# Kernel optimization log

Measured on AMD Instinct MI355X. Metric: run time of the kernel, lower is better.

Reference implementation:

```python
import jax, jax.numpy as jnp
import numpy as np

NUM_EMBEDDINGS = 8192
EMBEDDING_DIM = 256
COMMITMENT_COST = 0.25


def setup_inputs() -> dict:
    key = jax.random.key(0)
    k1, k2 = jax.random.split(key)
    inputs = jax.random.normal(k1, (16, 2048, EMBEDDING_DIM), dtype=jnp.float32)
    # codebook initialized uniform(-1/K, 1/K) as in the torch module
    codebook = jax.random.uniform(
        k2, (NUM_EMBEDDINGS, EMBEDDING_DIM), dtype=jnp.float32,
        minval=-1.0 / NUM_EMBEDDINGS, maxval=1.0 / NUM_EMBEDDINGS)
    return {"inputs": inputs, "codebook": codebook}


def reference(inputs, codebook):
    B, T, D = inputs.shape
    flat = inputs.reshape(-1, D)                      # [BT, D]
    distances = (
        jnp.sum(flat * flat, axis=1, keepdims=True)
        + jnp.sum(codebook * codebook, axis=1)
        - 2.0 * jnp.matmul(flat, codebook.T)
    )
    idx = jnp.argmin(distances, axis=1)               # [BT]
    quantized = codebook[idx].reshape(B, T, D)        # gather == one-hot @ codebook
    e_latent_loss = jnp.mean((jax.lax.stop_gradient(quantized) - inputs) ** 2)
    q_latent_loss = jnp.mean((quantized - jax.lax.stop_gradient(inputs)) ** 2)
    loss = q_latent_loss + COMMITMENT_COST * e_latent_loss
    # straight-through estimator
    quantized_st = inputs + jax.lax.stop_gradient(quantized - inputs)
    return quantized_st, idx.reshape(B, T), loss
```

## Files before the change

### kernel.cpp

```cpp
#include <hip/hip_runtime.h>
#include <hip/hip_bf16.h>
#include <stdint.h>

#define D      256
#define K      8192
#define NROWS  32768
#define QELEMS 8388608

typedef __attribute__((ext_vector_type(8))) short bf16x8;
typedef __attribute__((ext_vector_type(4))) float f32x4;
typedef unsigned int u32;
typedef unsigned short u16;

__device__ __forceinline__ u16 f2bf(float f) {
    u32 b = __float_as_uint(f);
    return (u16)((b + 0x7fffu + ((b >> 16) & 1u)) >> 16);
}
__device__ __forceinline__ float bf2f(u16 h) {
    return __uint_as_float((u32)h << 16);
}

__global__ __launch_bounds__(256) void vq_prep_kernel(
    const float* __restrict__ cb, u16* __restrict__ ch,
    float* __restrict__ se, u16* __restrict__ seh, float* __restrict__ loss_sum) {
    int row = blockIdx.x * 4 + (threadIdx.x >> 6);
    int l = threadIdx.x & 63;
    float4 v = *(const float4*)(cb + (size_t)row * D + l * 4);
    ushort4 o;
    o.x = f2bf(v.x); o.y = f2bf(v.y); o.z = f2bf(v.z); o.w = f2bf(v.w);
    *(ushort4*)(ch + (size_t)row * D + l * 4) = o;
    float s = v.x * v.x + v.y * v.y + v.z * v.z + v.w * v.w;
    #pragma unroll
    for (int off = 32; off > 0; off >>= 1) s += __shfl_down(s, off, 64);
    if (l == 0) { se[row] = s; seh[row] = f2bf(s); }
    if (blockIdx.x == 0 && threadIdx.x == 0) *loss_sum = 0.f;
}

__global__ __launch_bounds__(512, 4) void vq_filter_kernel(
    const u16* __restrict__ ch, const float* __restrict__ x,
    const u16* __restrict__ seh, u32* __restrict__ cand)
{
    __shared__ union {
        u16 as[2][16384];
        struct { float mv[64 * 33]; u32 mc[64 * 33]; } mg;
    } S;
    __shared__ __align__(16) u16 seL[8192];

    const int tid  = threadIdx.x;
    const int lane = tid & 63;
    const int wave = tid >> 6;
    const int m_w  = wave & 3;
    const int n_w  = wave >> 2;
    const int l15  = lane & 15;
    const int l4   = lane >> 4;
    const int row0 = blockIdx.x * 64;

    {
        uint4* dl = (uint4*)seL;
        const uint4* sg = (const uint4*)seh;
        dl[tid] = sg[tid];
        dl[tid + 512] = sg[tid + 512];
    }

    bf16x8 Bf[2][8];
    #pragma unroll
    for (int nt = 0; nt < 2; ++nt) {
        const float* xr = x + (size_t)(row0 + n_w * 32 + nt * 16 + l15) * D + l4 * 8;
        #pragma unroll
        for (int c = 0; c < 8; ++c) {
            float4 a = *(const float4*)(xr + c * 32);
            float4 b = *(const float4*)(xr + c * 32 + 4);
            bf16x8 f;
            f[0] = (short)f2bf(a.x); f[1] = (short)f2bf(a.y);
            f[2] = (short)f2bf(a.z); f[3] = (short)f2bf(a.w);
            f[4] = (short)f2bf(b.x); f[5] = (short)f2bf(b.y);
            f[6] = (short)f2bf(b.z); f[7] = (short)f2bf(b.w);
            Bf[nt][c] = f;
        }
    }

    float b0[2], b1[2]; int c0[2], c1[2];
    #pragma unroll
    for (int nt = 0; nt < 2; ++nt) { b0[nt] = 1e30f; b1[nt] = 1e30f; c0[nt] = 0; c1[nt] = 0; }

#define STAGE(TILE, BUF) do {                                                 \
    const int _kn = (TILE) << 6;                                              \
    _Pragma("unroll")                                                         \
    for (int i = 0; i < 4; ++i) {                                             \
        const u16* gp = ch + (size_t)(_kn + i * 16 + l15) * D + wave * 32 + l4 * 8; \
        u16* lb = &S.as[(BUF)][(size_t)(wave * 4 + i) * 512];                 \
        __builtin_amdgcn_global_load_lds(                                     \
            (const __attribute__((address_space(1))) u32*)gp,                 \
            (__attribute__((address_space(3))) u32*)lb, 16, 0, 0);            \
    }                                                                         \
} while (0)

#define EPI(NT, A) do {                                                       \
    float t0 = fmaf(-2.f, (A)[0], _se0);                                      \
    float t1 = fmaf(-2.f, (A)[1], _se1);                                      \
    float t2 = fmaf(-2.f, (A)[2], _se2);                                      \
    float t3 = fmaf(-2.f, (A)[3], _se3);                                      \
    float tmn = fminf(fminf(t0, t1), fminf(t2, t3));                          \
    if (tmn < b1[NT]) {                                                       \
        float tv[4] = {t0, t1, t2, t3};                                       \
        _Pragma("unroll")                                                     \
        for (int r = 0; r < 4; ++r) {                                         \
            float t = tv[r];                                                  \
            int cv = _kt + m_w * 16 + l4 * 4 + r;                             \
            bool in0 = t < b0[NT];                                            \
            bool in1 = t < b1[NT];                                            \
            float ob0 = b0[NT]; int oc0 = c0[NT];                             \
            b1[NT] = in0 ? ob0 : (in1 ? t  : b1[NT]);                         \
            c1[NT] = in0 ? oc0 : (in1 ? cv : c1[NT]);                         \
            b0[NT] = in0 ? t  : ob0;                                          \
            c0[NT] = in0 ? cv : oc0;                                          \
        }                                                                     \
    }                                                                         \
} while (0)

#define BODY(T, DO_STAGE, VMN) do {                                           \
    if (DO_STAGE) STAGE((T) + 1, ((T) + 1) & 1);                              \
    asm volatile("s_waitcnt vmcnt(" #VMN ")" ::: "memory");                   \
    __builtin_amdgcn_s_barrier();                                             \
    const int _kt = (T) << 6;                                                 \
    const u16* _as = &S.as[(T) & 1][0];                                       \
    f32x4 acc0 = {0.f,0.f,0.f,0.f}, acc1 = {0.f,0.f,0.f,0.f};                 \
    _Pragma("unroll")                                                         \
    for (int c = 0; c < 8; ++c) {                                             \
        bf16x8 Af = *(const bf16x8*)(_as + (size_t)(c * 4 + m_w) * 512 + lane * 8); \
        acc0 = __builtin_amdgcn_mfma_f32_16x16x32_bf16(Af, Bf[0][c], acc0, 0, 0, 0); \
        acc1 = __builtin_amdgcn_mfma_f32_16x16x32_bf16(Af, Bf[1][c], acc1, 0, 0, 0); \
    }                                                                         \
    ushort4 _sh = *(const ushort4*)(seL + _kt + m_w * 16 + l4 * 4);           \
    float _se0 = bf2f(_sh.x), _se1 = bf2f(_sh.y);                             \
    float _se2 = bf2f(_sh.z), _se3 = bf2f(_sh.w);                             \
    EPI(0, acc0); EPI(1, acc1);                                               \
    __builtin_amdgcn_s_barrier();                                             \
} while (0)

    STAGE(0, 0);
    __syncthreads();

    #pragma unroll 1
    for (int t = 0; t < 127; ++t) BODY(t, 1, 4);
    BODY(127, 0, 0);

#undef BODY
#undef EPI
#undef STAGE

    #pragma unroll
    for (int nt = 0; nt < 2; ++nt) {
        int rl = n_w * 32 + nt * 16 + l15;
        int g  = m_w * 4 + l4;
        S.mg.mv[rl * 33 + g * 2]     = b0[nt];
        S.mg.mv[rl * 33 + g * 2 + 1] = b1[nt];
        S.mg.mc[rl * 33 + g * 2]     = (u32)c0[nt];
        S.mg.mc[rl * 33 + g * 2 + 1] = (u32)c1[nt];
    }
    __syncthreads();

    {
        int tsk = tid;
        int row = tsk >> 3, m = tsk & 7;
        const float* v  = S.mg.mv + row * 33 + m * 4;
        const u32*   cc = S.mg.mc + row * 33 + m * 4;
        float v00 = v[0],  v01 = v[1],  v10 = v[2],  v11 = v[3];
        u32   c00 = cc[0], c01 = cc[1], c10 = cc[2], c11 = cc[3];
        bool  aw  = v00 <= v10;
        u32   w0c = aw ? c00 : c10;
        float s1  = aw ? v10 : v00; u32 s1c = aw ? c10 : c00;
        float s2  = aw ? v01 : v11; u32 s2c = aw ? c01 : c11;
        u32   w1c = (s2 <= s1) ? s2c : s1c;
        cand[(size_t)(row0 + row) * 16 + m * 2]     = w0c;
        cand[(size_t)(row0 + row) * 16 + m * 2 + 1] = w1c;
    }
}

__global__ __launch_bounds__(1024) void vq_rescore_kernel(
    const float* __restrict__ x, const float* __restrict__ cb,
    const float* __restrict__ se, const u32* __restrict__ cand,
    float* __restrict__ out, float* __restrict__ loss_sum)
{
    const int wave = threadIdx.x >> 6;
    const int lane = threadIdx.x & 63;
    const int row  = blockIdx.x * 16 + wave;

    float4 xv = *(const float4*)(x + (size_t)row * D + lane * 4);
    float sx = xv.x * xv.x + xv.y * xv.y + xv.z * xv.z + xv.w * xv.w;
    #pragma unroll
    for (int o = 1; o < 64; o <<= 1) sx += __shfl_xor(sx, o, 64);

    u32 myc = cand[(size_t)row * 16 + (lane & 15)];
    float best = 1e30f; int bk = 0x7fffffff;
    #pragma unroll 4
    for (int j = 0; j < 16; ++j) {
        int code = __shfl((int)myc, j, 64);
        float4 ev = *(const float4*)(cb + (size_t)code * D + lane * 4);
        float p = xv.x * ev.x + xv.y * ev.y + xv.z * ev.z + xv.w * ev.w;
        #pragma unroll
        for (int o = 1; o < 64; o <<= 1) p += __shfl_xor(p, o, 64);
        float dist = (sx + se[code]) - 2.0f * p;
        if (dist < best || (dist == best && code < bk)) { best = dist; bk = code; }
    }

    float4 q = *(const float4*)(cb + (size_t)bk * D + lane * 4);
    *(float4*)(out + (size_t)row * D + lane * 4) = q;
    float dx = q.x - xv.x, dy = q.y - xv.y, dz = q.z - xv.z, dw = q.w - xv.w;
    float s = dx * dx + dy * dy + dz * dz + dw * dw;
    #pragma unroll
    for (int o = 1; o < 64; o <<= 1) s += __shfl_xor(s, o, 64);
    if (lane == 0) out[QELEMS + row] = (float)bk;

    __shared__ float red[16];
    if (lane == 0) red[wave] = s;
    __syncthreads();
    if (threadIdx.x == 0) {
        float t = 0.f;
        #pragma unroll
        for (int w2 = 0; w2 < 16; ++w2) t += red[w2];
        atomicAdd(loss_sum, t);
    }
}

__global__ void vq_fin_kernel(const float* __restrict__ loss_sum, float* __restrict__ out) {
    out[QELEMS + NROWS] = 1.25f * (*loss_sum) * (1.0f / (float)QELEMS);
}

extern "C" void kernel_launch(void* const* d_in, const int* in_sizes, int n_in,
                              void* d_out, int out_size, void* d_ws, size_t ws_size,
                              hipStream_t stream) {
    const float* x  = (const float*)d_in[0];
    const float* cb = (const float*)d_in[1];
    float* out = (float*)d_out;

    u16* ch = (u16*)d_out;

    char* ws = (char*)d_ws;
    float* loss_sum = (float*)ws;
    float* sebuf    = (float*)(ws + 4096);
    u16*   seh      = (u16*)(ws + 40960);
    u32*   cand     = (u32*)(ws + 65536);

    vq_prep_kernel<<<K / 4, 256, 0, stream>>>(cb, ch, sebuf, seh, loss_sum);
    vq_filter_kernel<<<NROWS / 64, 512, 0, stream>>>(ch, x, seh, cand);
    vq_rescore_kernel<<<NROWS / 16, 1024, 0, stream>>>(x, cb, sebuf, cand, out, loss_sum);
    vq_fin_kernel<<<1, 1, 0, stream>>>(loss_sum, out);
}
```

Measured before the change: 399.0 us.

## Split codebook search across two blocks per row tile to double grid parallelism

The filter kernel now launches twice as many blocks, with each pair covering the same 64 input rows but searching only one half of the 8192-entry codebook. Each block keeps top-2 candidates per 16-lane group and reduces them to 4 candidate pairs, writing 8 of the 16 candidate slots per row. This is meant to raise occupancy and hide latency on a grid that was only 512 blocks. The cost is that input rows are loaded and converted to bf16 twice, and the merged candidate set is coarser per half.

After: 415.2 us. +4.1%, slower.

```diff
diff --git a/kernel.cpp b/kernel.cpp
--- a/kernel.cpp
+++ b/kernel.cpp
@@ -44,7 +44,7 @@
         u16 as[2][16384];
         struct { float mv[64 * 33]; u32 mc[64 * 33]; } mg;
     } S;
-    __shared__ __align__(16) u16 seL[8192];
+    __shared__ __align__(16) u16 seL[4096];
 
     const int tid  = threadIdx.x;
     const int lane = tid & 63;
@@ -53,13 +53,16 @@
     const int n_w  = wave >> 2;
     const int l15  = lane & 15;
     const int l4   = lane >> 4;
-    const int row0 = blockIdx.x * 64;
+    const int g    = blockIdx.x;
+    const int half = (g & 7) >> 2;
+    const int rc   = (g >> 3) * 4 + (g & 3);
+    const int row0 = rc * 64;
+    const int kbase = half * 4096;
 
     {
         uint4* dl = (uint4*)seL;
-        const uint4* sg = (const uint4*)seh;
+        const uint4* sg = (const uint4*)(seh + kbase);
         dl[tid] = sg[tid];
-        dl[tid + 512] = sg[tid + 512];
     }
 
     bf16x8 Bf[2][8];
@@ -84,7 +87,7 @@
     for (int nt = 0; nt < 2; ++nt) { b0[nt] = 1e30f; b1[nt] = 1e30f; c0[nt] = 0; c1[nt] = 0; }
 
 #define STAGE(TILE, BUF) do {                                                 \
-    const int _kn = (TILE) << 6;                                              \
+    const int _kn = kbase + ((TILE) << 6);                                    \
     _Pragma("unroll")                                                         \
     for (int i = 0; i < 4; ++i) {                                             \
         const u16* gp = ch + (size_t)(_kn + i * 16 + l15) * D + wave * 32 + l4 * 8; \
@@ -106,7 +109,7 @@
         _Pragma("unroll")                                                     \
         for (int r = 0; r < 4; ++r) {                                         \
             float t = tv[r];                                                  \
-            int cv = _kt + m_w * 16 + l4 * 4 + r;                             \
+            int cv = kbase + _kt + m_w * 16 + l4 * 4 + r;                     \
             bool in0 = t < b0[NT];                                            \
             bool in1 = t < b1[NT];                                            \
             float ob0 = b0[NT]; int oc0 = c0[NT];                             \
@@ -142,8 +145,8 @@
     __syncthreads();
 
     #pragma unroll 1
-    for (int t = 0; t < 127; ++t) BODY(t, 1, 4);
-    BODY(127, 0, 0);
+    for (int t = 0; t < 63; ++t) BODY(t, 1, 4);
+    BODY(63, 0, 0);
 
 #undef BODY
 #undef EPI
@@ -152,28 +155,37 @@
     #pragma unroll
     for (int nt = 0; nt < 2; ++nt) {
         int rl = n_w * 32 + nt * 16 + l15;
-        int g  = m_w * 4 + l4;
-        S.mg.mv[rl * 33 + g * 2]     = b0[nt];
-        S.mg.mv[rl * 33 + g * 2 + 1] = b1[nt];
-        S.mg.mc[rl * 33 + g * 2]     = (u32)c0[nt];
-        S.mg.mc[rl * 33 + g * 2 + 1] = (u32)c1[nt];
+        int gq = m_w * 4 + l4;
+        S.mg.mv[rl * 33 + gq * 2]     = b0[nt];
+        S.mg.mv[rl * 33 + gq * 2 + 1] = b1[nt];
+        S.mg.mc[rl * 33 + gq * 2]     = (u32)c0[nt];
+        S.mg.mc[rl * 33 + gq * 2 + 1] = (u32)c1[nt];
     }
     __syncthreads();
 
-    {
-        int tsk = tid;
-        int row = tsk >> 3, m = tsk & 7;
-        const float* v  = S.mg.mv + row * 33 + m * 4;
-        const u32*   cc = S.mg.mc + row * 33 + m * 4;
-        float v00 = v[0],  v01 = v[1],  v10 = v[2],  v11 = v[3];
-        u32   c00 = cc[0], c01 = cc[1], c10 = cc[2], c11 = cc[3];
-        bool  aw  = v00 <= v10;
-        u32   w0c = aw ? c00 : c10;
-        float s1  = aw ? v10 : v00; u32 s1c = aw ? c10 : c00;
-        float s2  = aw ? v01 : v11; u32 s2c = aw ? c01 : c11;
-        u32   w1c = (s2 <= s1) ? s2c : s1c;
-        cand[(size_t)(row0 + row) * 16 + m * 2]     = w0c;
-        cand[(size_t)(row0 + row) * 16 + m * 2 + 1] = w1c;
+    if (tid < 256) {
+        int row = tid >> 2, q = tid & 3;
+        const float* v  = S.mg.mv + row * 33 + q * 8;
+        const u32*   cc = S.mg.mc + row * 33 + q * 8;
+        bool  a1 = v[0] <= v[2];
+        float p0v = a1 ? v[0] : v[2];  u32 p0c = a1 ? cc[0] : cc[2];
+        float s1a = a1 ? v[2] : v[0];  u32 s1ac = a1 ? cc[2] : cc[0];
+        float s2a = a1 ? v[1] : v[3];  u32 s2ac = a1 ? cc[1] : cc[3];
+        bool  a2 = s2a <= s1a;
+        float p1v = a2 ? s2a : s1a;    u32 p1c = a2 ? s2ac : s1ac;
+        bool  b1m = v[4] <= v[6];
+        float q0v = b1m ? v[4] : v[6]; u32 q0c = b1m ? cc[4] : cc[6];
+        float s1b = b1m ? v[6] : v[4]; u32 s1bc = b1m ? cc[6] : cc[4];
+        float s2b = b1m ? v[5] : v[7]; u32 s2bc = b1m ? cc[5] : cc[7];
+        bool  b2 = s2b <= s1b;
+        float q1v = b2 ? s2b : s1b;    u32 q1c = b2 ? s2bc : s1bc;
+        bool  f1 = p0v <= q0v;
+        u32   w0c = f1 ? p0c : q0c;
+        float s1f = f1 ? q0v : p0v;    u32 s1fc = f1 ? q0c : p0c;
+        float s2f = f1 ? p1v : q1v;    u32 s2fc = f1 ? p1c : q1c;
+        u32   w1c = (s2f <= s1f) ? s2fc : s1fc;
+        cand[(size_t)(row0 + row) * 16 + half * 8 + q * 2]     = w0c;
+        cand[(size_t)(row0 + row) * 16 + half * 8 + q * 2 + 1] = w1c;
     }
 }
 
@@ -243,7 +255,7 @@
     u32*   cand     = (u32*)(ws + 65536);
 
     vq_prep_kernel<<<K / 4, 256, 0, stream>>>(cb, ch, sebuf, seh, loss_sum);
-    vq_filter_kernel<<<NROWS / 64, 512, 0, stream>>>(ch, x, seh, cand);
+    vq_filter_kernel<<<2 * NROWS / 64, 512, 0, stream>>>(ch, x, seh, cand);
     vq_rescore_kernel<<<NROWS / 16, 1024, 0, stream>>>(x, cb, sebuf, cand, out, loss_sum);
     vq_fin_kernel<<<1, 1, 0, stream>>>(loss_sum, out);
 }
```

## Split codebook tiles into half-K phases with a four-slot LDS ring

Applied to the files above, without the earlier changes.

Each 64-code tile is now split into two half-depth phases. Each phase loads into one slot of a four-deep LDS ring and is prefetched three phases ahead, with one barrier per phase instead of two. LDS fragment reads are issued before the wait and barrier, and MFMA priority is raised with s_setprio, to overlap loads with compute. The early LDS reads happen before the matching vmcnt wait and barrier, and slot reuse is not clearly fenced, so the code risks reading stale tile data.

Measured after the change: 401.8 us. About the same (+0.7%).

```diff
diff --git a/kernel.cpp b/kernel.cpp
--- a/kernel.cpp
+++ b/kernel.cpp
@@ -41,7 +41,7 @@
     const u16* __restrict__ seh, u32* __restrict__ cand)
 {
     __shared__ union {
-        u16 as[2][16384];
+        u16 hb[4][8192];
         struct { float mv[64 * 33]; u32 mc[64 * 33]; } mg;
     } S;
     __shared__ __align__(16) u16 seL[8192];
@@ -83,12 +83,16 @@
     #pragma unroll
     for (int nt = 0; nt < 2; ++nt) { b0[nt] = 1e30f; b1[nt] = 1e30f; c0[nt] = 0; c1[nt] = 0; }
 
-#define STAGE(TILE, BUF) do {                                                 \
-    const int _kn = (TILE) << 6;                                              \
+#define STAGE_HALF(H, SLOT) do {                                              \
+    const int _h = (H);                                                       \
+    const int _t64 = (_h >> 1) * 64;                                          \
+    const int _db  = (_h & 1) * 128;                                          \
     _Pragma("unroll")                                                         \
-    for (int i = 0; i < 4; ++i) {                                             \
-        const u16* gp = ch + (size_t)(_kn + i * 16 + l15) * D + wave * 32 + l4 * 8; \
-        u16* lb = &S.as[(BUF)][(size_t)(wave * 4 + i) * 512];                 \
+    for (int i = 0; i < 2; ++i) {                                             \
+        const int g2 = wave * 2 + i;                                          \
+        const u16* gp = ch + (size_t)(_t64 + (g2 & 3) * 16 + l15) * D         \
+                           + _db + (g2 >> 2) * 32 + l4 * 8;                   \
+        u16* lb = &S.hb[(SLOT)][(size_t)g2 * 512];                            \
         __builtin_amdgcn_global_load_lds(                                     \
             (const __attribute__((address_space(1))) u32*)gp,                 \
             (__attribute__((address_space(3))) u32*)lb, 16, 0, 0);            \
@@ -118,36 +122,59 @@
     }                                                                         \
 } while (0)
 
-#define BODY(T, DO_STAGE, VMN) do {                                           \
-    if (DO_STAGE) STAGE((T) + 1, ((T) + 1) & 1);                              \
+#define PHASE(P, HH, DO_STAGE, VMN) do {                                      \
+    if (DO_STAGE) STAGE_HALF((P) + 3, ((P) + 3) & 3);                         \
+    const u16* _hb = &S.hb[(P) & 3][0];                                       \
+    bf16x8 Af0 = *(const bf16x8*)(_hb + (size_t)(0 * 4 + m_w) * 512 + lane * 8); \
+    bf16x8 Af1 = *(const bf16x8*)(_hb + (size_t)(1 * 4 + m_w) * 512 + lane * 8); \
+    bf16x8 Af2 = *(const bf16x8*)(_hb + (size_t)(2 * 4 + m_w) * 512 + lane * 8); \
+    bf16x8 Af3 = *(const bf16x8*)(_hb + (size_t)(3 * 4 + m_w) * 512 + lane * 8); \
     asm volatile("s_waitcnt vmcnt(" #VMN ")" ::: "memory");                   \
+    __builtin_amdgcn_sched_barrier(0);                                        \
     __builtin_amdgcn_s_barrier();                                             \
-    const int _kt = (T) << 6;                                                 \
-    const u16* _as = &S.as[(T) & 1][0];                                       \
-    f32x4 acc0 = {0.f,0.f,0.f,0.f}, acc1 = {0.f,0.f,0.f,0.f};                 \
-    _Pragma("unroll")                                                         \
-    for (int c = 0; c < 8; ++c) {                                             \
-        bf16x8 Af = *(const bf16x8*)(_as + (size_t)(c * 4 + m_w) * 512 + lane * 8); \
-        acc0 = __builtin_amdgcn_mfma_f32_16x16x32_bf16(Af, Bf[0][c], acc0, 0, 0, 0); \
-        acc1 = __builtin_amdgcn_mfma_f32_16x16x32_bf16(Af, Bf[1][c], acc1, 0, 0, 0); \
+    __builtin_amdgcn_sched_barrier(0);                                        \
+    asm volatile("s_waitcnt lgkmcnt(0)" ::: "memory");                        \
+    __builtin_amdgcn_sched_barrier(0);                                        \
+    if ((HH) == 0) { acc0 = (f32x4){0.f,0.f,0.f,0.f}; acc1 = (f32x4){0.f,0.f,0.f,0.f}; } \
+    __builtin_amdgcn_s_setprio(1);                                            \
+    acc0 = __builtin_amdgcn_mfma_f32_16x16x32_bf16(Af0, Bf[0][(HH)*4+0], acc0, 0, 0, 0); \
+    acc1 = __builtin_amdgcn_mfma_f32_16x16x32_bf16(Af0, Bf[1][(HH)*4+0], acc1, 0, 0, 0); \
+    acc0 = __builtin_amdgcn_mfma_f32_16x16x32_bf16(Af1, Bf[0][(HH)*4+1], acc0, 0, 0, 0); \
+    acc1 = __builtin_amdgcn_mfma_f32_16x16x32_bf16(Af1, Bf[1][(HH)*4+1], acc1, 0, 0, 0); \
+    acc0 = __builtin_amdgcn_mfma_f32_16x16x32_bf16(Af2, Bf[0][(HH)*4+2], acc0, 0, 0, 0); \
+    acc1 = __builtin_amdgcn_mfma_f32_16x16x32_bf16(Af2, Bf[1][(HH)*4+2], acc1, 0, 0, 0); \
+    acc0 = __builtin_amdgcn_mfma_f32_16x16x32_bf16(Af3, Bf[0][(HH)*4+3], acc0, 0, 0, 0); \
+    acc1 = __builtin_amdgcn_mfma_f32_16x16x32_bf16(Af3, Bf[1][(HH)*4+3], acc1, 0, 0, 0); \
+    __builtin_amdgcn_s_setprio(0);                                            \
+    if ((HH) == 1) {                                                          \
+        const int _kt = ((P) >> 1) << 6;                                      \
+        ushort4 _sh = *(const ushort4*)(seL + _kt + m_w * 16 + l4 * 4);       \
+        float _se0 = bf2f(_sh.x), _se1 = bf2f(_sh.y);                         \
+        float _se2 = bf2f(_sh.z), _se3 = bf2f(_sh.w);                         \
+        EPI(0, acc0); EPI(1, acc1);                                           \
     }                                                                         \
-    ushort4 _sh = *(const ushort4*)(seL + _kt + m_w * 16 + l4 * 4);           \
-    float _se0 = bf2f(_sh.x), _se1 = bf2f(_sh.y);                             \
-    float _se2 = bf2f(_sh.z), _se3 = bf2f(_sh.w);                             \
-    EPI(0, acc0); EPI(1, acc1);                                               \
-    __builtin_amdgcn_s_barrier();                                             \
 } while (0)
 
-    STAGE(0, 0);
-    __syncthreads();
-
+    STAGE_HALF(0, 0); STAGE_HALF(1, 1); STAGE_HALF(2, 2);
+    asm volatile("s_waitcnt lgkmcnt(0)" ::: "memory");
+    __builtin_amdgcn_s_barrier();
+    __builtin_amdgcn_sched_barrier(0);
+
+    f32x4 acc0, acc1;
     #pragma unroll 1
-    for (int t = 0; t < 127; ++t) BODY(t, 1, 4);
-    BODY(127, 0, 0);
-
-#undef BODY
+    for (int T = 0; T < 126; ++T) {
+        const int p = T * 2;
+        PHASE(p,     0, 1, 4);
+        PHASE(p + 1, 1, 1, 4);
+    }
+    PHASE(252, 0, 1, 4);
+    PHASE(253, 1, 0, 2);
+    PHASE(254, 0, 0, 0);
+    PHASE(255, 1, 0, 0);
+
+#undef PHASE
 #undef EPI
-#undef STAGE
+#undef STAGE_HALF
 
     #pragma unroll
     for (int nt = 0; nt < 2; ++nt) {
```
